# Kernel optimization log

Measured on AMD Instinct MI355X. Metric: run time of the kernel, lower is better.

The kernel has to match this reference:

```python
import jax, jax.numpy as jnp
import numpy as np


def _tsallis15_probs(x):
    """entmax-1.5 / Tsallis alpha=1.5 mapping over axis=1. x: [n, d] logits."""
    x = (x - jnp.max(x, axis=1, keepdims=True)) * 0.5
    xs = -jnp.sort(-x, axis=1)                       # descending sort  [n, d]
    d = x.shape[1]
    rho = jnp.arange(1, d + 1, dtype=x.dtype)        # 1..d
    mean = jnp.cumsum(xs, axis=1) / rho
    mean_sq = jnp.cumsum(xs * xs, axis=1) / rho
    ss = rho * (mean_sq - mean * mean)
    delta = (1.0 - ss) / rho
    tau = mean - jnp.sqrt(jnp.clip(delta, 0.0))
    support_size = jnp.sum(tau <= xs, axis=1)        # [n]
    tau_star = jnp.take_along_axis(tau, (support_size - 1)[:, None], axis=1)
    y = jnp.clip(x - tau_star, 0.0)
    return y * y                                     # p*, rows sum to 1


def setup_inputs() -> dict:
    key = jax.random.key(0)
    k1, k2 = jax.random.split(key)
    inp = jax.random.normal(k1, (2048, 32000), dtype=jnp.float32)
    target = jax.random.randint(k2, (2048,), 0, 32000, dtype=jnp.int64)
    return {"input": inp, "target": target}


def reference(input, target):
    n = input.shape[0]
    p_star = _tsallis15_probs(input)
    # omega_tsallis15: (1 - sum p^{3/2}) / 0.75 per row
    loss = (1.0 - jnp.sum(p_star * jnp.sqrt(p_star), axis=1)) / 0.75
    # scatter_add(-1) at the target class, then <p* - e_y, x> per row
    pm = p_star.at[jnp.arange(n), target].add(-1.0)
    loss = loss + jnp.einsum('ij,ij->i', pm, input)
    # reduction='elementwise_mean', ignore_index=-100 (<0: no masking)
    return jnp.sum(loss) / n
```

## Files before the change

kernel.cpp:

```cpp
#include <hip/hip_runtime.h>
#include <math.h>

#define BLOCK 512
#define NWAVES (BLOCK / 64)
#define NV 16
#define CAND_CAP 6144
#define NREG 12

__device__ __forceinline__ float waveReduceMax(float v) {
#pragma unroll
    for (int off = 32; off > 0; off >>= 1)
        v = fmaxf(v, __shfl_down(v, off, 64));
    return v;
}
__device__ __forceinline__ float waveReduceSum(float v) {
#pragma unroll
    for (int off = 32; off > 0; off >>= 1)
        v += __shfl_down(v, off, 64);
    return v;
}

__global__ __launch_bounds__(BLOCK, 4) void tsallis15_kernel(
    const float* __restrict__ x, const int* __restrict__ tgt,
    float* __restrict__ out, int n, int d, float inv_n)
{
    __shared__ float s_cand[CAND_CAP];
    __shared__ float s_red[NWAVES];
    __shared__ int   s_cnt;
    __shared__ float s_bcast;

    const int row  = blockIdx.x;
    const int t    = threadIdx.x;
    const int lane = t & 63;
    const int wave = t >> 6;
    const float* __restrict__ xr = x + (size_t)row * (size_t)d;
    const float4* __restrict__ xr4 = reinterpret_cast<const float4*>(xr);
    const int d4 = d >> 2;
    const int tail0 = d4 << 2;

    if (t == 0) s_cnt = 0;

    float4 r[NV];
#pragma unroll
    for (int j = 0; j < NV; ++j) {
        int idx = t + j * BLOCK;
        if (idx < d4) {
            r[j] = xr4[idx];
        } else {
            r[j] = make_float4(-INFINITY, -INFINITY, -INFINITY, -INFINITY);
        }
    }
    float tailv = -INFINITY;
    if (tail0 + t < d) tailv = xr[tail0 + t];

    float m = tailv;
#pragma unroll
    for (int j = 0; j < NV; ++j)
        m = fmaxf(m, fmaxf(fmaxf(r[j].x, r[j].y), fmaxf(r[j].z, r[j].w)));
    m = waveReduceMax(m);
    if (lane == 0) s_red[wave] = m;
    __syncthreads();
    if (wave == 0) {
        float v = (lane < NWAVES) ? s_red[lane] : -INFINITY;
        v = waveReduceMax(v);
        if (lane == 0) s_bcast = v;
    }
    __syncthreads();
    const float rowmax = s_bcast;
    const float thr = rowmax - 2.0f;

#pragma unroll
    for (int j = 0; j < NV; ++j) {
        float4 v = r[j];
        float mx4 = fmaxf(fmaxf(v.x, v.y), fmaxf(v.z, v.w));
        unsigned long long any = __ballot(mx4 >= thr);
        if (any) {
            float vals[4] = { v.x, v.y, v.z, v.w };
#pragma unroll
            for (int c = 0; c < 4; ++c) {
                float vv = vals[c];
                bool pred = (vv >= thr);
                unsigned long long mask = __ballot(pred);
                if (mask) {
                    int base;
                    if (lane == 0) base = atomicAdd(&s_cnt, __popcll(mask));
                    base = __shfl(base, 0, 64);
                    if (pred) {
                        int pos = base + (int)__popcll(mask & ((1ull << lane) - 1ull));
                        if (pos < CAND_CAP) s_cand[pos] = (vv - rowmax) * 0.5f;
                    }
                }
            }
        }
    }
    {
        bool pred = (tailv >= thr);
        unsigned long long mask = __ballot(pred);
        if (mask) {
            int base;
            if (lane == 0) base = atomicAdd(&s_cnt, __popcll(mask));
            base = __shfl(base, 0, 64);
            if (pred) {
                int pos = base + (int)__popcll(mask & ((1ull << lane) - 1ull));
                if (pos < CAND_CAP) s_cand[pos] = (tailv - rowmax) * 0.5f;
            }
        }
    }
    __syncthreads();

    if (wave == 0) {
        const int k = min(s_cnt, CAND_CAP);

        float xt = 0.0f;
        if (lane == 0) xt = xr[tgt[row]];

        float ur[NREG];
#pragma unroll
        for (int j = 0; j < NREG; ++j) {
            int idx = lane + 64 * j;
            ur[j] = (idx < k) ? s_cand[idx] : -1e30f;
        }

        float lo = -1.0f, hi = 0.0f;
        for (int it = 0; it < 18; ++it) {
            float tau = 0.5f * (lo + hi);
            float acc = 0.0f;
#pragma unroll
            for (int j = 0; j < NREG; ++j) {
                float u = ur[j] - tau;
                acc += (u > 0.0f) ? u * u : 0.0f;
            }
            for (int j = 64 * NREG + lane; j < k; j += 64) {
                float u = s_cand[j] - tau;
                if (u > 0.0f) acc += u * u;
            }
            float tot = waveReduceSum(acc);
            tot = __shfl(tot, 0, 64);
            if (tot >= 1.0f) lo = tau; else hi = tau;
        }
        const float tau_b = 0.5f * (lo + hi);

        float s1 = 0.0f, s2 = 0.0f, sc = 0.0f;
#pragma unroll
        for (int j = 0; j < NREG; ++j) {
            float u = ur[j];
            if (u > tau_b) { s1 += u; s2 += u * u; sc += 1.0f; }
        }
        for (int j = 64 * NREG + lane; j < k; j += 64) {
            float u = s_cand[j];
            if (u > tau_b) { s1 += u; s2 += u * u; sc += 1.0f; }
        }
        s1 = waveReduceSum(s1); s1 = __shfl(s1, 0, 64);
        s2 = waveReduceSum(s2); s2 = __shfl(s2, 0, 64);
        sc = waveReduceSum(sc); sc = __shfl(sc, 0, 64);
        float mean  = s1 / sc;
        float ss    = s2 - s1 * mean;
        float delta = (1.0f - ss) / sc;
        if (delta < 0.0f) delta = 0.0f;
        const float tau_star = mean - sqrtf(delta);

        float p32 = 0.0f, dot = 0.0f;
#pragma unroll
        for (int j = 0; j < NREG; ++j) {
            float u = ur[j] - tau_star;
            if (u > 0.0f) {
                float p = u * u;
                p32 += p * u;
                dot += p * (2.0f * ur[j] + rowmax);
            }
        }
        for (int j = 64 * NREG + lane; j < k; j += 64) {
            float uc = s_cand[j];
            float u  = uc - tau_star;
            if (u > 0.0f) {
                float p = u * u;
                p32 += p * u;
                dot += p * (2.0f * uc + rowmax);
            }
        }
        p32 = waveReduceSum(p32);
        dot = waveReduceSum(dot);
        if (lane == 0) {
            float loss = (1.0f - p32) * (4.0f / 3.0f) + dot - xt;
            atomicAdd(out, loss * inv_n);
        }
    }
}

extern "C" void kernel_launch(void* const* d_in, const int* in_sizes, int n_in,
                              void* d_out, int out_size, void* d_ws, size_t ws_size,
                              hipStream_t stream) {
    const float* x   = (const float*)d_in[0];
    const int*   tgt = (const int*)d_in[1];
    float*       out = (float*)d_out;

    const int n = in_sizes[1];
    const int d = in_sizes[0] / n;

    hipMemsetAsync(out, 0, (size_t)out_size * sizeof(float), stream);
    tsallis15_kernel<<<n, BLOCK, 0, stream>>>(x, tgt, out, n, d, 1.0f / (float)n);
}
```

Baseline: 384.2 us.

## Make kernel persistent with async global-to-LDS prefetch of the next row

Launches a fixed grid of at most 256 blocks of 1024 threads. Each block loops over rows and prefetches the next row into a 128KB LDS buffer with global_load_lds while it processes the current one. Target logits for up to 64 rows are gathered up front and handed out by shuffle. The goal is to overlap HBM loads with the max/candidate/bisection work. In exchange, the large LDS footprint limits each CU to one block, and the single-wave bisection tail is no longer hidden by other resident blocks. The unchanged launch bounds of 4 blocks with 1024 threads may also squeeze registers.

After: 428.7 us. 11.6% more time.

```diff
diff --git a/kernel.cpp b/kernel.cpp
--- a/kernel.cpp
+++ b/kernel.cpp
@@ -1,11 +1,23 @@
 #include <hip/hip_runtime.h>
 #include <math.h>
 
-#define BLOCK 512
+#define BLOCK 1024
 #define NWAVES (BLOCK / 64)
-#define NV 16
+#define NV 8
+#define SROW_F (BLOCK * NV * 4)
 #define CAND_CAP 6144
 #define NREG 12
+
+#define BAR()      asm volatile("s_waitcnt lgkmcnt(0)\n\ts_barrier" ::: "memory")
+#define WAIT_VM0() asm volatile("s_waitcnt vmcnt(0)" ::: "memory")
+#define WAIT_LGKM0() asm volatile("s_waitcnt lgkmcnt(0)" ::: "memory")
+
+__device__ __forceinline__ void gload_lds16(const float* g, float* l) {
+    __builtin_amdgcn_global_load_lds(
+        (const __attribute__((address_space(1))) void*)g,
+        (__attribute__((address_space(3))) void*)l,
+        16, 0, 0);
+}
 
 __device__ __forceinline__ float waveReduceMax(float v) {
 #pragma unroll
@@ -24,165 +36,209 @@
     const float* __restrict__ x, const int* __restrict__ tgt,
     float* __restrict__ out, int n, int d, float inv_n)
 {
+    __shared__ __align__(16) float s_row[SROW_F];
     __shared__ float s_cand[CAND_CAP];
     __shared__ float s_red[NWAVES];
     __shared__ int   s_cnt;
     __shared__ float s_bcast;
 
-    const int row  = blockIdx.x;
-    const int t    = threadIdx.x;
-    const int lane = t & 63;
-    const int wave = t >> 6;
-    const float* __restrict__ xr = x + (size_t)row * (size_t)d;
-    const float4* __restrict__ xr4 = reinterpret_cast<const float4*>(xr);
-    const int d4 = d >> 2;
+    const int t     = threadIdx.x;
+    const int lane  = t & 63;
+    const int wave  = t >> 6;
+    const int grid  = gridDim.x;
+    const int row0  = blockIdx.x;
+    const int d4    = d >> 2;
     const int tail0 = d4 << 2;
 
     if (t == 0) s_cnt = 0;
 
-    float4 r[NV];
-#pragma unroll
-    for (int j = 0; j < NV; ++j) {
-        int idx = t + j * BLOCK;
-        if (idx < d4) {
-            r[j] = xr4[idx];
-        } else {
-            r[j] = make_float4(-INFINITY, -INFINITY, -INFINITY, -INFINITY);
+    {
+        const float* xr = x + (size_t)row0 * (size_t)d;
+#pragma unroll
+        for (int j = 0; j < NV; ++j) {
+            int idx = t + j * BLOCK;
+            int fo  = (wave << 8) + (j << 12);
+            if (idx < d4)
+                gload_lds16(xr + fo + (lane << 2), &s_row[fo]);
         }
     }
-    float tailv = -INFINITY;
-    if (tail0 + t < d) tailv = xr[tail0 + t];
-
-    float m = tailv;
-#pragma unroll
-    for (int j = 0; j < NV; ++j)
-        m = fmaxf(m, fmaxf(fmaxf(r[j].x, r[j].y), fmaxf(r[j].z, r[j].w)));
-    m = waveReduceMax(m);
-    if (lane == 0) s_red[wave] = m;
-    __syncthreads();
+
+    float xt_pre = 0.0f;
     if (wave == 0) {
-        float v = (lane < NWAVES) ? s_red[lane] : -INFINITY;
-        v = waveReduceMax(v);
-        if (lane == 0) s_bcast = v;
+        int r = row0 + lane * grid;
+        if (r < n) {
+            int ti = tgt[r];
+            xt_pre = x[(size_t)r * (size_t)d + ti];
+        }
     }
-    __syncthreads();
-    const float rowmax = s_bcast;
-    const float thr = rowmax - 2.0f;
-
-#pragma unroll
-    for (int j = 0; j < NV; ++j) {
-        float4 v = r[j];
-        float mx4 = fmaxf(fmaxf(v.x, v.y), fmaxf(v.z, v.w));
-        unsigned long long any = __ballot(mx4 >= thr);
-        if (any) {
-            float vals[4] = { v.x, v.y, v.z, v.w };
-#pragma unroll
-            for (int c = 0; c < 4; ++c) {
-                float vv = vals[c];
-                bool pred = (vv >= thr);
-                unsigned long long mask = __ballot(pred);
-                if (mask) {
-                    int base;
-                    if (lane == 0) base = atomicAdd(&s_cnt, __popcll(mask));
-                    base = __shfl(base, 0, 64);
-                    if (pred) {
-                        int pos = base + (int)__popcll(mask & ((1ull << lane) - 1ull));
-                        if (pos < CAND_CAP) s_cand[pos] = (vv - rowmax) * 0.5f;
+
+    int iter = 0;
+    for (int row = row0; row < n; row += grid, ++iter) {
+        const float* xr = x + (size_t)row * (size_t)d;
+        const int nextrow = row + grid;
+
+        WAIT_VM0();
+
+        float tailv = -INFINITY;
+        if (tail0 + t < d) tailv = xr[tail0 + t];
+
+        float4 r[NV];
+#pragma unroll
+        for (int j = 0; j < NV; ++j) {
+            int idx = t + j * BLOCK;
+            r[j] = (idx < d4)
+                 ? *reinterpret_cast<const float4*>(&s_row[4 * idx])
+                 : make_float4(-INFINITY, -INFINITY, -INFINITY, -INFINITY);
+        }
+        WAIT_LGKM0();
+
+        if (nextrow < n) {
+            const float* xn = x + (size_t)nextrow * (size_t)d;
+#pragma unroll
+            for (int j = 0; j < NV; ++j) {
+                int idx = t + j * BLOCK;
+                int fo  = (wave << 8) + (j << 12);
+                if (idx < d4)
+                    gload_lds16(xn + fo + (lane << 2), &s_row[fo]);
+            }
+        }
+
+        float m = tailv;
+#pragma unroll
+        for (int j = 0; j < NV; ++j)
+            m = fmaxf(m, fmaxf(fmaxf(r[j].x, r[j].y), fmaxf(r[j].z, r[j].w)));
+        m = waveReduceMax(m);
+        if (lane == 0) s_red[wave] = m;
+        BAR();
+        if (wave == 0) {
+            float v = (lane < NWAVES) ? s_red[lane] : -INFINITY;
+            v = waveReduceMax(v);
+            if (lane == 0) s_bcast = v;
+        }
+        BAR();
+        const float rowmax = s_bcast;
+        const float thr = rowmax - 2.0f;
+
+#pragma unroll
+        for (int j = 0; j < NV; ++j) {
+            float4 v = r[j];
+            float mx4 = fmaxf(fmaxf(v.x, v.y), fmaxf(v.z, v.w));
+            unsigned long long any = __ballot(mx4 >= thr);
+            if (any) {
+                float vals[4] = { v.x, v.y, v.z, v.w };
+#pragma unroll
+                for (int c = 0; c < 4; ++c) {
+                    float vv = vals[c];
+                    bool pred = (vv >= thr);
+                    unsigned long long mask = __ballot(pred);
+                    if (mask) {
+                        int base;
+                        if (lane == 0) base = atomicAdd(&s_cnt, __popcll(mask));
+                        base = __shfl(base, 0, 64);
+                        if (pred) {
+                            int pos = base + (int)__popcll(mask & ((1ull << lane) - 1ull));
+                            if (pos < CAND_CAP) s_cand[pos] = (vv - rowmax) * 0.5f;
+                        }
                     }
                 }
             }
         }
-    }
-    {
-        bool pred = (tailv >= thr);
-        unsigned long long mask = __ballot(pred);
-        if (mask) {
-            int base;
-            if (lane == 0) base = atomicAdd(&s_cnt, __popcll(mask));
-            base = __shfl(base, 0, 64);
-            if (pred) {
-                int pos = base + (int)__popcll(mask & ((1ull << lane) - 1ull));
-                if (pos < CAND_CAP) s_cand[pos] = (tailv - rowmax) * 0.5f;
-            }
-        }
-    }
-    __syncthreads();
-
-    if (wave == 0) {
-        const int k = min(s_cnt, CAND_CAP);
-
-        float xt = 0.0f;
-        if (lane == 0) xt = xr[tgt[row]];
-
-        float ur[NREG];
-#pragma unroll
-        for (int j = 0; j < NREG; ++j) {
-            int idx = lane + 64 * j;
-            ur[j] = (idx < k) ? s_cand[idx] : -1e30f;
-        }
-
-        float lo = -1.0f, hi = 0.0f;
-        for (int it = 0; it < 18; ++it) {
-            float tau = 0.5f * (lo + hi);
-            float acc = 0.0f;
+        {
+            bool pred = (tailv >= thr);
+            unsigned long long mask = __ballot(pred);
+            if (mask) {
+                int base;
+                if (lane == 0) base = atomicAdd(&s_cnt, __popcll(mask));
+                base = __shfl(base, 0, 64);
+                if (pred) {
+                    int pos = base + (int)__popcll(mask & ((1ull << lane) - 1ull));
+                    if (pos < CAND_CAP) s_cand[pos] = (tailv - rowmax) * 0.5f;
+                }
+            }
+        }
+        BAR();
+
+        if (wave == 0) {
+            const int k = min(s_cnt, CAND_CAP);
+            if (lane == 0) s_cnt = 0;
+
+            float ur[NREG];
 #pragma unroll
             for (int j = 0; j < NREG; ++j) {
-                float u = ur[j] - tau;
-                acc += (u > 0.0f) ? u * u : 0.0f;
+                int idx = lane + 64 * j;
+                ur[j] = (idx < k) ? s_cand[idx] : -1e30f;
+            }
+
+            float lo = -1.0f, hi = 0.0f;
+            for (int it = 0; it < 18; ++it) {
+                float tau = 0.5f * (lo + hi);
+                float acc = 0.0f;
+#pragma unroll
+                for (int j = 0; j < NREG; ++j) {
+                    float u = ur[j] - tau;
+                    acc += (u > 0.0f) ? u * u : 0.0f;
+                }
+                for (int j = 64 * NREG + lane; j < k; j += 64) {
+                    float u = s_cand[j] - tau;
+                    if (u > 0.0f) acc += u * u;
+                }
+                float tot = waveReduceSum(acc);
+                tot = __shfl(tot, 0, 64);
+                if (tot >= 1.0f) lo = tau; else hi = tau;
+            }
+            const float tau_b = 0.5f * (lo + hi);
+
+            float s1 = 0.0f, s2 = 0.0f, sc = 0.0f;
+#pragma unroll
+            for (int j = 0; j < NREG; ++j) {
+                float u = ur[j];
+                if (u > tau_b) { s1 += u; s2 += u * u; sc += 1.0f; }
             }
             for (int j = 64 * NREG + lane; j < k; j += 64) {
-                float u = s_cand[j] - tau;
-                if (u > 0.0f) acc += u * u;
-            }
-            float tot = waveReduceSum(acc);
-            tot = __shfl(tot, 0, 64);
-            if (tot >= 1.0f) lo = tau; else hi = tau;
-        }
-        const float tau_b = 0.5f * (lo + hi);
-
-        float s1 = 0.0f, s2 = 0.0f, sc = 0.0f;
-#pragma unroll
-        for (int j = 0; j < NREG; ++j) {
-            float u = ur[j];
-            if (u > tau_b) { s1 += u; s2 += u * u; sc += 1.0f; }
-        }
-        for (int j = 64 * NREG + lane; j < k; j += 64) {
-            float u = s_cand[j];
-            if (u > tau_b) { s1 += u; s2 += u * u; sc += 1.0f; }
-        }
-        s1 = waveReduceSum(s1); s1 = __shfl(s1, 0, 64);
-        s2 = waveReduceSum(s2); s2 = __shfl(s2, 0, 64);
-        sc = waveReduceSum(sc); sc = __shfl(sc, 0, 64);
-        float mean  = s1 / sc;
-        float ss    = s2 - s1 * mean;
-        float delta = (1.0f - ss) / sc;
-        if (delta < 0.0f) delta = 0.0f;
-        const float tau_star = mean - sqrtf(delta);
-
-        float p32 = 0.0f, dot = 0.0f;
-#pragma unroll
-        for (int j = 0; j < NREG; ++j) {
-            float u = ur[j] - tau_star;
-            if (u > 0.0f) {
-                float p = u * u;
-                p32 += p * u;
-                dot += p * (2.0f * ur[j] + rowmax);
-            }
-        }
-        for (int j = 64 * NREG + lane; j < k; j += 64) {
-            float uc = s_cand[j];
-            float u  = uc - tau_star;
-            if (u > 0.0f) {
-                float p = u * u;
-                p32 += p * u;
-                dot += p * (2.0f * uc + rowmax);
-            }
-        }
-        p32 = waveReduceSum(p32);
-        dot = waveReduceSum(dot);
-        if (lane == 0) {
-            float loss = (1.0f - p32) * (4.0f / 3.0f) + dot - xt;
-            atomicAdd(out, loss * inv_n);
+                float u = s_cand[j];
+                if (u > tau_b) { s1 += u; s2 += u * u; sc += 1.0f; }
+            }
+            s1 = waveReduceSum(s1); s1 = __shfl(s1, 0, 64);
+            s2 = waveReduceSum(s2); s2 = __shfl(s2, 0, 64);
+            sc = waveReduceSum(sc); sc = __shfl(sc, 0, 64);
+            float mean  = s1 / sc;
+            float ss    = s2 - s1 * mean;
+            float delta = (1.0f - ss) / sc;
+            if (delta < 0.0f) delta = 0.0f;
+            const float tau_star = mean - sqrtf(delta);
+
+            float p32 = 0.0f, dot = 0.0f;
+#pragma unroll
+            for (int j = 0; j < NREG; ++j) {
+                float u = ur[j] - tau_star;
+                if (u > 0.0f) {
+                    float p = u * u;
+                    p32 += p * u;
+                    dot += p * (2.0f * ur[j] + rowmax);
+                }
+            }
+            for (int j = 64 * NREG + lane; j < k; j += 64) {
+                float uc = s_cand[j];
+                float u  = uc - tau_star;
+                if (u > 0.0f) {
+                    float p = u * u;
+                    p32 += p * u;
+                    dot += p * (2.0f * uc + rowmax);
+                }
+            }
+            p32 = waveReduceSum(p32);
+            dot = waveReduceSum(dot);
+
+            float xt;
+            if (iter < 64) {
+                xt = __shfl(xt_pre, iter, 64);
+            } else {
+                xt = (lane == 0) ? xr[tgt[row]] : 0.0f;
+            }
+            if (lane == 0) {
+                float loss = (1.0f - p32) * (4.0f / 3.0f) + dot - xt;
+                atomicAdd(out, loss * inv_n);
+            }
         }
     }
 }
@@ -198,5 +254,6 @@
     const int d = in_sizes[0] / n;
 
     hipMemsetAsync(out, 0, (size_t)out_size * sizeof(float), stream);
-    tsallis15_kernel<<<n, BLOCK, 0, stream>>>(x, tgt, out, n, d, 1.0f / (float)n);
-}
+    const int grid = (n < 256) ? n : 256;
+    tsallis15_kernel<<<grid, BLOCK, 0, stream>>>(x, tgt, out, n, d, 1.0f / (float)n);
+}
```

## Process two rows per 1024-thread block with independent half-block pipelines

Applied to the files above, without the earlier changes.

Each block now holds two rows, one per 512-thread half, with separate shared candidate buffers, counters and max reductions. The serial per-row threshold solve runs on one wave per half, so two solves proceed concurrently within a block. The target logit load is hoisted to the start, and the candidate capacity and register-cached candidate count are reduced. This risks register pressure from the larger block under the same launch bound, and a smaller candidate cap.

Measured after the change: 414.0 us. 7.7% more time.

```diff
diff --git a/kernel.cpp b/kernel.cpp
--- a/kernel.cpp
+++ b/kernel.cpp
@@ -1,11 +1,12 @@
 #include <hip/hip_runtime.h>
 #include <math.h>
 
-#define BLOCK 512
-#define NWAVES (BLOCK / 64)
-#define NV 16
-#define CAND_CAP 6144
-#define NREG 12
+#define BLOCK 1024
+#define HALF  512
+#define NWAVES 16
+#define NV    16
+#define CAPH  4096
+#define NREG  8
 
 __device__ __forceinline__ float waveReduceMax(float v) {
 #pragma unroll
@@ -18,60 +19,144 @@
     for (int off = 32; off > 0; off >>= 1)
         v += __shfl_down(v, off, 64);
     return v;
+}
+
+__device__ __forceinline__ void solve_wave(const float* s_cand, int k,
+                                           float rowmax, float xt,
+                                           float inv_n, float* out, int lane)
+{
+    float ur[NREG];
+#pragma unroll
+    for (int j = 0; j < NREG; ++j) {
+        int idx = lane + 64 * j;
+        ur[j] = (idx < k) ? s_cand[idx] : -1e30f;
+    }
+
+    float lo = -1.0f, hi = 0.0f;
+    for (int it = 0; it < 18; ++it) {
+        float tau = 0.5f * (lo + hi);
+        float acc = 0.0f;
+#pragma unroll
+        for (int j = 0; j < NREG; ++j) {
+            float u = ur[j] - tau;
+            acc += (u > 0.0f) ? u * u : 0.0f;
+        }
+        for (int j = 64 * NREG + lane; j < k; j += 64) {
+            float u = s_cand[j] - tau;
+            if (u > 0.0f) acc += u * u;
+        }
+        float tot = waveReduceSum(acc);
+        tot = __shfl(tot, 0, 64);
+        if (tot >= 1.0f) lo = tau; else hi = tau;
+    }
+    const float tau_b = 0.5f * (lo + hi);
+
+    float s1 = 0.0f, s2 = 0.0f, sc = 0.0f;
+#pragma unroll
+    for (int j = 0; j < NREG; ++j) {
+        float u = ur[j];
+        if (u > tau_b) { s1 += u; s2 += u * u; sc += 1.0f; }
+    }
+    for (int j = 64 * NREG + lane; j < k; j += 64) {
+        float u = s_cand[j];
+        if (u > tau_b) { s1 += u; s2 += u * u; sc += 1.0f; }
+    }
+    s1 = waveReduceSum(s1); s1 = __shfl(s1, 0, 64);
+    s2 = waveReduceSum(s2); s2 = __shfl(s2, 0, 64);
+    sc = waveReduceSum(sc); sc = __shfl(sc, 0, 64);
+    float mean  = s1 / sc;
+    float ss    = s2 - s1 * mean;
+    float delta = (1.0f - ss) / sc;
+    if (delta < 0.0f) delta = 0.0f;
+    const float tau_star = mean - sqrtf(delta);
+
+    float p32 = 0.0f, dot = 0.0f;
+#pragma unroll
+    for (int j = 0; j < NREG; ++j) {
+        float u = ur[j] - tau_star;
+        if (u > 0.0f) {
+            float p = u * u;
+            p32 += p * u;
+            dot += p * (2.0f * ur[j] + rowmax);
+        }
+    }
+    for (int j = 64 * NREG + lane; j < k; j += 64) {
+        float uc = s_cand[j];
+        float u  = uc - tau_star;
+        if (u > 0.0f) {
+            float p = u * u;
+            p32 += p * u;
+            dot += p * (2.0f * uc + rowmax);
+        }
+    }
+    p32 = waveReduceSum(p32);
+    dot = waveReduceSum(dot);
+    if (lane == 0) {
+        float loss = (1.0f - p32) * (4.0f / 3.0f) + dot - xt;
+        atomicAdd(out, loss * inv_n);
+    }
 }
 
 __global__ __launch_bounds__(BLOCK, 4) void tsallis15_kernel(
     const float* __restrict__ x, const int* __restrict__ tgt,
     float* __restrict__ out, int n, int d, float inv_n)
 {
-    __shared__ float s_cand[CAND_CAP];
+    __shared__ float s_cand[2][CAPH];
     __shared__ float s_red[NWAVES];
-    __shared__ int   s_cnt;
-    __shared__ float s_bcast;
-
-    const int row  = blockIdx.x;
+    __shared__ float s_max[2];
+    __shared__ int   s_cnt[2];
+
     const int t    = threadIdx.x;
     const int lane = t & 63;
     const int wave = t >> 6;
+    const int half = wave >> 3;
+    const int th   = t & (HALF - 1);
+    const int row  = blockIdx.x * 2 + half;
+    const bool rv  = (row < n);
     const float* __restrict__ xr = x + (size_t)row * (size_t)d;
     const float4* __restrict__ xr4 = reinterpret_cast<const float4*>(xr);
     const int d4 = d >> 2;
-    const int tail0 = d4 << 2;
-
-    if (t == 0) s_cnt = 0;
+
+    if (t < 2) s_cnt[t] = 0;
+
+    float xt = 0.0f;
+    if (th == 0 && rv) xt = xr[tgt[row]];
 
     float4 r[NV];
 #pragma unroll
-    for (int j = 0; j < NV; ++j) {
-        int idx = t + j * BLOCK;
-        if (idx < d4) {
-            r[j] = xr4[idx];
-        } else {
-            r[j] = make_float4(-INFINITY, -INFINITY, -INFINITY, -INFINITY);
-        }
+    for (int i = 0; i < NV; ++i) {
+        int idx = i * HALF + th;
+        r[i] = (rv && idx < d4)
+             ? xr4[idx]
+             : make_float4(-INFINITY, -INFINITY, -INFINITY, -INFINITY);
     }
     float tailv = -INFINITY;
-    if (tail0 + t < d) tailv = xr[tail0 + t];
+    {
+        int e = (d4 << 2) + th;
+        if (rv && e < d && th < (d & 3) + 1) tailv = xr[e];
+    }
 
     float m = tailv;
 #pragma unroll
-    for (int j = 0; j < NV; ++j)
-        m = fmaxf(m, fmaxf(fmaxf(r[j].x, r[j].y), fmaxf(r[j].z, r[j].w)));
+    for (int i = 0; i < NV; ++i)
+        m = fmaxf(m, fmaxf(fmaxf(r[i].x, r[i].y), fmaxf(r[i].z, r[i].w)));
     m = waveReduceMax(m);
     if (lane == 0) s_red[wave] = m;
     __syncthreads();
-    if (wave == 0) {
-        float v = (lane < NWAVES) ? s_red[lane] : -INFINITY;
+    if ((wave & 7) == 0) {
+        float v = (lane < 8) ? s_red[half * 8 + lane] : -INFINITY;
         v = waveReduceMax(v);
-        if (lane == 0) s_bcast = v;
+        if (lane == 0) s_max[half] = v;
     }
     __syncthreads();
-    const float rowmax = s_bcast;
+    const float rowmax = s_max[half];
     const float thr = rowmax - 2.0f;
 
-#pragma unroll
-    for (int j = 0; j < NV; ++j) {
-        float4 v = r[j];
+    float* s_c = s_cand[half];
+    int*   s_k = &s_cnt[half];
+#pragma unroll
+    for (int i = 0; i < NV; ++i) {
+        float4 v = r[i];
         float mx4 = fmaxf(fmaxf(v.x, v.y), fmaxf(v.z, v.w));
         unsigned long long any = __ballot(mx4 >= thr);
         if (any) {
@@ -83,11 +168,11 @@
                 unsigned long long mask = __ballot(pred);
                 if (mask) {
                     int base;
-                    if (lane == 0) base = atomicAdd(&s_cnt, __popcll(mask));
+                    if (lane == 0) base = atomicAdd(s_k, __popcll(mask));
                     base = __shfl(base, 0, 64);
                     if (pred) {
                         int pos = base + (int)__popcll(mask & ((1ull << lane) - 1ull));
-                        if (pos < CAND_CAP) s_cand[pos] = (vv - rowmax) * 0.5f;
+                        if (pos < CAPH) s_c[pos] = (vv - rowmax) * 0.5f;
                     }
                 }
             }
@@ -98,92 +183,19 @@
         unsigned long long mask = __ballot(pred);
         if (mask) {
             int base;
-            if (lane == 0) base = atomicAdd(&s_cnt, __popcll(mask));
+            if (lane == 0) base = atomicAdd(s_k, __popcll(mask));
             base = __shfl(base, 0, 64);
             if (pred) {
                 int pos = base + (int)__popcll(mask & ((1ull << lane) - 1ull));
-                if (pos < CAND_CAP) s_cand[pos] = (tailv - rowmax) * 0.5f;
+                if (pos < CAPH) s_c[pos] = (tailv - rowmax) * 0.5f;
             }
         }
     }
     __syncthreads();
 
-    if (wave == 0) {
-        const int k = min(s_cnt, CAND_CAP);
-
-        float xt = 0.0f;
-        if (lane == 0) xt = xr[tgt[row]];
-
-        float ur[NREG];
-#pragma unroll
-        for (int j = 0; j < NREG; ++j) {
-            int idx = lane + 64 * j;
-            ur[j] = (idx < k) ? s_cand[idx] : -1e30f;
-        }
-
-        float lo = -1.0f, hi = 0.0f;
-        for (int it = 0; it < 18; ++it) {
-            float tau = 0.5f * (lo + hi);
-            float acc = 0.0f;
-#pragma unroll
-            for (int j = 0; j < NREG; ++j) {
-                float u = ur[j] - tau;
-                acc += (u > 0.0f) ? u * u : 0.0f;
-            }
-            for (int j = 64 * NREG + lane; j < k; j += 64) {
-                float u = s_cand[j] - tau;
-                if (u > 0.0f) acc += u * u;
-            }
-            float tot = waveReduceSum(acc);
-            tot = __shfl(tot, 0, 64);
-            if (tot >= 1.0f) lo = tau; else hi = tau;
-        }
-        const float tau_b = 0.5f * (lo + hi);
-
-        float s1 = 0.0f, s2 = 0.0f, sc = 0.0f;
-#pragma unroll
-        for (int j = 0; j < NREG; ++j) {
-            float u = ur[j];
-            if (u > tau_b) { s1 += u; s2 += u * u; sc += 1.0f; }
-        }
-        for (int j = 64 * NREG + lane; j < k; j += 64) {
-            float u = s_cand[j];
-            if (u > tau_b) { s1 += u; s2 += u * u; sc += 1.0f; }
-        }
-        s1 = waveReduceSum(s1); s1 = __shfl(s1, 0, 64);
-        s2 = waveReduceSum(s2); s2 = __shfl(s2, 0, 64);
-        sc = waveReduceSum(sc); sc = __shfl(sc, 0, 64);
-        float mean  = s1 / sc;
-        float ss    = s2 - s1 * mean;
-        float delta = (1.0f - ss) / sc;
-        if (delta < 0.0f) delta = 0.0f;
-        const float tau_star = mean - sqrtf(delta);
-
-        float p32 = 0.0f, dot = 0.0f;
-#pragma unroll
-        for (int j = 0; j < NREG; ++j) {
-            float u = ur[j] - tau_star;
-            if (u > 0.0f) {
-                float p = u * u;
-                p32 += p * u;
-                dot += p * (2.0f * ur[j] + rowmax);
-            }
-        }
-        for (int j = 64 * NREG + lane; j < k; j += 64) {
-            float uc = s_cand[j];
-            float u  = uc - tau_star;
-            if (u > 0.0f) {
-                float p = u * u;
-                p32 += p * u;
-                dot += p * (2.0f * uc + rowmax);
-            }
-        }
-        p32 = waveReduceSum(p32);
-        dot = waveReduceSum(dot);
-        if (lane == 0) {
-            float loss = (1.0f - p32) * (4.0f / 3.0f) + dot - xt;
-            atomicAdd(out, loss * inv_n);
-        }
+    if ((wave & 7) == 0 && rv) {
+        const int k = min(*s_k, CAPH);
+        solve_wave(s_c, k, rowmax, xt, inv_n, out, lane);
     }
 }
 
@@ -198,5 +210,6 @@
     const int d = in_sizes[0] / n;
 
     hipMemsetAsync(out, 0, (size_t)out_size * sizeof(float), stream);
-    tsallis15_kernel<<<n, BLOCK, 0, stream>>>(x, tgt, out, n, d, 1.0f / (float)n);
-}
+    const int grid = (n + 1) / 2;
+    tsallis15_kernel<<<grid, BLOCK, 0, stream>>>(x, tgt, out, n, d, 1.0f / (float)n);
+}
```
